# Kernel tuning notes

Measured on AMD Instinct MI355X. Metric: run time of the kernel, lower is better.

The kernel has to match this reference:

```python
import jax, jax.numpy as jnp
import numpy as np

B_SZ, SEQ, D_IN, D_ST, D_OUT = 16, 8192, 128, 128, 128


def setup_inputs() -> dict:
    key = jax.random.key(0)
    ku, ka, kb, kc, kd = jax.random.split(key, 5)
    u = jax.random.normal(ku, (B_SZ, SEQ, D_IN), dtype=jnp.float32)
    # A scaled to spectral radius ~0.9 so the long recurrence stays stable
    A = jax.random.normal(ka, (D_ST, D_ST), dtype=jnp.float32) * (0.9 / np.sqrt(D_ST))
    B = jax.random.normal(kb, (D_ST, D_IN), dtype=jnp.float32) * (1.0 / np.sqrt(D_IN))
    C = jax.random.normal(kc, (D_OUT, D_ST), dtype=jnp.float32) * (1.0 / np.sqrt(D_ST))
    D = jax.random.normal(kd, (D_OUT, D_IN), dtype=jnp.float32) * (1.0 / np.sqrt(D_IN))
    return {"u": u, "A": A, "B": B, "C": C, "D": D}


def reference(u, A, B, C, D):
    # x_t = x_{t-1} A^T + u_t B^T ; y_t = x_t C^T + u_t D^T ; x_0 = 0
    batch = u.shape[0]
    state0 = jnp.zeros((batch, A.shape[0]), dtype=u.dtype)

    def step(state, u_t):  # state: [B, S_dim], u_t: [B, D_in]
        new_state = state @ A.T + u_t @ B.T
        y = new_state @ C.T + u_t @ D.T
        return new_state, y

    u_t_first = jnp.swapaxes(u, 0, 1)  # [SEQ, B, D_in]
    _, ys = jax.lax.scan(step, state0, u_t_first)
    return jnp.swapaxes(ys, 0, 1)  # [B, SEQ, D_out]
```

## Files before the change

### kernel.cpp

```cpp
#include <hip/hip_runtime.h>


#define SEQ 8192
#define BS  16
#define DD  128
#define CL  16
#define NC  512
#define GRP 16
#define NG  32

typedef __bf16 bf16t;
typedef __bf16 bf16x8 __attribute__((ext_vector_type(8)));
typedef __bf16 bf16x4 __attribute__((ext_vector_type(4)));
typedef float  f32x4  __attribute__((ext_vector_type(4)));

#define MFMA(a,b,c) __builtin_amdgcn_mfma_f32_16x16x32_bf16(a,b,c,0,0,0)

__device__ __forceinline__ int swz(int b, int j) { return j ^ ((b & 7) << 3); }

struct Frag  { bf16x8 h[4]; bf16x8 l[4]; };
struct FragH { bf16x8 h[4]; };

__device__ __forceinline__ void load_frag_T(const float* __restrict__ src, int lane, int w, Frag& f) {
    int n  = (w << 4) + (lane & 15);
    int kb = ((lane >> 4) & 3) << 3;
#pragma unroll
    for (int q = 0; q < 4; q++) {
        const float* p = src + n * DD + (q << 5) + kb;
#pragma unroll
        for (int e = 0; e < 8; e++) {
            float v = p[e];
            bf16t hh = (bf16t)v;
            f.h[q][e] = hh;
            f.l[q][e] = (bf16t)(v - (float)hh);
        }
    }
}

__device__ __forceinline__ void load_frag_T_h(const float* __restrict__ src, int lane, int w, FragH& f) {
    int n  = (w << 4) + (lane & 15);
    int kb = ((lane >> 4) & 3) << 3;
#pragma unroll
    for (int q = 0; q < 4; q++) {
        const float* p = src + n * DD + (q << 5) + kb;
#pragma unroll
        for (int e = 0; e < 8; e++) f.h[q][e] = (bf16t)p[e];
    }
}

__device__ __forceinline__ void load_frag_N(const float* __restrict__ src, int lane, int w, Frag& f) {
    int n  = (w << 4) + (lane & 15);
    int kb = ((lane >> 4) & 3) << 3;
#pragma unroll
    for (int q = 0; q < 4; q++) {
#pragma unroll
        for (int e = 0; e < 8; e++) {
            float v = src[((q << 5) + kb + e) * DD + n];
            bf16t hh = (bf16t)v;
            f.h[q][e] = hh;
            f.l[q][e] = (bf16t)(v - (float)hh);
        }
    }
}

__device__ __forceinline__ bf16x8 afrag(const bf16t* __restrict__ X, int lane, int q) {
    int b  = lane & 15;
    int j0 = (q << 5) + (((lane >> 4) & 3) << 3);
    return *(const bf16x8*)(X + b * DD + swz(b, j0));
}

__device__ __forceinline__ void put_state(bf16t* __restrict__ H, bf16t* __restrict__ L,
                                          int lane, int w, f32x4 acc) {
    int n = (w << 4) + (lane & 15);
#pragma unroll
    for (int r = 0; r < 4; r++) {
        int b = (((lane >> 4) & 3) << 2) + r;
        float v = acc[r];
        bf16t hh = (bf16t)v;
        H[b * DD + swz(b, n)] = hh;
        L[b * DD + swz(b, n)] = (bf16t)(v - (float)hh);
    }
}

__device__ __forceinline__ void stage_rows(const float* __restrict__ src, long rs,
                                           bf16t* __restrict__ H, bf16t* __restrict__ L, int tid) {
    int b  = tid >> 5;
    int j0 = (tid & 31) << 2;
    float4 v = *(const float4*)(src + (long)b * rs + j0);
    float vv[4] = { v.x, v.y, v.z, v.w };
    bf16x4 h, l;
#pragma unroll
    for (int e = 0; e < 4; e++) {
        bf16t hh = (bf16t)vv[e];
        h[e] = hh;
        l[e] = (bf16t)(vv[e] - (float)hh);
    }
    *(bf16x4*)(H + b * DD + swz(b, j0)) = h;
    *(bf16x4*)(L + b * DD + swz(b, j0)) = l;
}

__device__ __forceinline__ void write_u_h(bf16t* __restrict__ H, int b_, int j0_, float4 v) {
    float vv[4] = { v.x, v.y, v.z, v.w };
    bf16x4 h;
#pragma unroll
    for (int e = 0; e < 4; e++) h[e] = (bf16t)vv[e];
    *(bf16x4*)(H + b_ * DD + swz(b_, j0_)) = h;
}

__device__ __forceinline__ f32x4 load_accfrag(const float* __restrict__ src, int lane, int w) {
    int n = (w << 4) + (lane & 15);
    f32x4 a;
#pragma unroll
    for (int r = 0; r < 4; r++) {
        int b = (((lane >> 4) & 3) << 2) + r;
        a[r] = src[b * DD + n];
    }
    return a;
}

__device__ __forceinline__ void store_accfrag(float* __restrict__ dst, int lane, int w,
                                              f32x4 a, long rs) {
    int n = (w << 4) + (lane & 15);
#pragma unroll
    for (int r = 0; r < 4; r++) {
        int b = (((lane >> 4) & 3) << 2) + r;
        dst[(long)b * rs + n] = a[r];
    }
}

__global__ __launch_bounds__(128) void k_prepGH(const float* __restrict__ A,
                                                const float* __restrict__ B,
                                                const float* __restrict__ C,
                                                const float* __restrict__ D,
                                                float* __restrict__ Gm, float* __restrict__ Hm) {
    int sel = blockIdx.x >> 7, r = blockIdx.x & 127, j = threadIdx.x;
    const float* R = sel ? B : A;
    float s = 0.f;
#pragma unroll 8
    for (int m = 0; m < 128; m++) s = fmaf(C[r * 128 + m], R[m * 128 + j], s);
    if (sel) Hm[r * 128 + j] = s + D[r * 128 + j];
    else     Gm[r * 128 + j] = s;
}

__global__ __launch_bounds__(512, 4) void k_chunk(const float* __restrict__ u,
                                                  const float* __restrict__ A,
                                                  const float* __restrict__ Bm,
                                                  float* __restrict__ E,
                                                  float* __restrict__ P) {
    __shared__ __align__(16) bf16t Xh[2][BS * DD], Xl[2][BS * DD];
    __shared__ __align__(16) bf16t Uh[2][BS * DD];
    int tid = threadIdx.x, lane = tid & 63, w = tid >> 6;
    bool ident = blockIdx.x < 8;
    int g2 = blockIdx.x, c = blockIdx.x - 8;

    Frag fA; FragH fB;
    load_frag_T(A, lane, w, fA);
    if (!ident) load_frag_T_h(Bm, lane, w, fB);

    for (int i = tid; i < BS * DD; i += 512) {
        int b = i >> 7, j = swz(b, i & 127);
        Xh[0][i] = (bf16t)((ident && j == g2 * 16 + b) ? 1.f : 0.f);
        Xl[0][i] = (bf16t)0.f;
    }
    const float* ubase = u + (long)c * CL * DD;
    int b_ = tid >> 5, j0_ = (tid & 31) << 2;
    if (!ident) {
        float4 v0 = *(const float4*)(ubase + (long)b_ * SEQ * DD + j0_);
        write_u_h(Uh[0], b_, j0_, v0);
    }
    __syncthreads();

    int p = 0;
    f32x4 acc = {0.f, 0.f, 0.f, 0.f};
    for (int i = 0; i < CL; i++) {
        float4 un = {0, 0, 0, 0};
        if (!ident && i + 1 < CL)
            un = *(const float4*)(ubase + (long)b_ * SEQ * DD + (i + 1) * DD + j0_);
        f32x4 ax = {0,0,0,0}, ax2 = {0,0,0,0};
#pragma unroll
        for (int q = 0; q < 4; q++) {
            bf16x8 xh = afrag(Xh[p], lane, q), xl = afrag(Xl[p], lane, q);
            ax  = MFMA(xh, fA.h[q], ax);
            ax2 = MFMA(xl, fA.h[q], ax2);
            ax2 = MFMA(xh, fA.l[q], ax2);
            if (!ident) {
                bf16x8 uh = afrag(Uh[i & 1], lane, q);
                ax = MFMA(uh, fB.h[q], ax);
            }
        }
        acc = ax + ax2;
        if (i + 1 < CL) {
            put_state(Xh[p ^ 1], Xl[p ^ 1], lane, w, acc);
            if (!ident) write_u_h(Uh[(i + 1) & 1], b_, j0_, un);
            __syncthreads();
            p ^= 1;
        }
    }
    if (!ident) store_accfrag(E + (long)c * BS * DD, lane, w, acc, DD);
    else        store_accfrag(P + (long)g2 * 16 * DD, lane, w, acc, DD);
}

__global__ __launch_bounds__(512) void k_group(const float* __restrict__ E,
                                               const float* __restrict__ P,
                                               float* __restrict__ E2,
                                               float* __restrict__ Pg) {
    __shared__ __align__(16) bf16t Xh[2][BS * DD], Xl[2][BS * DD];
    int tid = threadIdx.x, lane = tid & 63, w = tid >> 6;
    bool ident = blockIdx.x >= NG;
    int g2 = blockIdx.x - NG;
    Frag fP;
    load_frag_N(P, lane, w, fP);
    for (int i = tid; i < BS * DD; i += 512) {
        int b = i >> 7, j = swz(b, i & 127);
        Xh[0][i] = (bf16t)((ident && j == g2 * 16 + b) ? 1.f : 0.f);
        Xl[0][i] = (bf16t)0.f;
    }
    __syncthreads();
    int p = 0, g = blockIdx.x;
    f32x4 acc = {0.f, 0.f, 0.f, 0.f};
    for (int r = 0; r < GRP; r++) {
        f32x4 a1 = {0.f,0.f,0.f,0.f}, a2 = {0.f,0.f,0.f,0.f};
        if (!ident) a1 = load_accfrag(E + (long)(g * GRP + r) * BS * DD, lane, w);
#pragma unroll
        for (int q = 0; q < 4; q++) {
            bf16x8 xh = afrag(Xh[p], lane, q), xl = afrag(Xl[p], lane, q);
            a1 = MFMA(xh, fP.h[q], a1);
            a2 = MFMA(xl, fP.h[q], a2);
            a1 = MFMA(xh, fP.l[q], a1);
        }
        acc = a1 + a2;
        if (r + 1 < GRP) {
            put_state(Xh[p ^ 1], Xl[p ^ 1], lane, w, acc);
            __syncthreads();
            p ^= 1;
        }
    }
    if (!ident) store_accfrag(E2 + (long)g * BS * DD, lane, w, acc, DD);
    else        store_accfrag(Pg + (long)g2 * 16 * DD, lane, w, acc, DD);
}

__global__ __launch_bounds__(512) void k_top(const float* __restrict__ E2,
                                             const float* __restrict__ Pg,
                                             float* __restrict__ S2) {
    __shared__ __align__(16) bf16t Xh[2][BS * DD], Xl[2][BS * DD];
    int tid = threadIdx.x, lane = tid & 63, w = tid >> 6;
    Frag fP;
    load_frag_N(Pg, lane, w, fP);
    for (int i = tid; i < BS * DD; i += 512) {
        Xh[0][i] = (bf16t)0.f;
        Xl[0][i] = (bf16t)0.f;
    }
    __syncthreads();
    int p = 0;
    f32x4 T = {0.f, 0.f, 0.f, 0.f};
    f32x4 e2 = load_accfrag(E2, lane, w);
    for (int g = 0; g < NG; g++) {
        store_accfrag(S2 + (long)g * BS * DD, lane, w, T, DD);
        if (g + 1 == NG) break;
        f32x4 e2n = load_accfrag(E2 + (long)(g + 1) * BS * DD, lane, w);
        f32x4 a1 = e2, a2 = {0.f,0.f,0.f,0.f};
#pragma unroll
        for (int q = 0; q < 4; q++) {
            bf16x8 xh = afrag(Xh[p], lane, q), xl = afrag(Xl[p], lane, q);
            a1 = MFMA(xh, fP.h[q], a1);
            a2 = MFMA(xl, fP.h[q], a2);
            a1 = MFMA(xh, fP.l[q], a1);
        }
        T = a1 + a2;
        put_state(Xh[p ^ 1], Xl[p ^ 1], lane, w, T);
        __syncthreads();
        p ^= 1;
        e2 = e2n;
    }
}

__global__ __launch_bounds__(512) void k_fix(float* __restrict__ E,
                                             const float* __restrict__ P,
                                             const float* __restrict__ S2) {
    __shared__ __align__(16) bf16t Xh[2][BS * DD], Xl[2][BS * DD];
    int tid = threadIdx.x, lane = tid & 63, w = tid >> 6;
    int g = blockIdx.x;
    Frag fP;
    load_frag_N(P, lane, w, fP);
    stage_rows(S2 + (long)g * BS * DD, DD, Xh[0], Xl[0], tid);
    f32x4 T = load_accfrag(S2 + (long)g * BS * DD, lane, w);
    __syncthreads();
    int p = 0;
    for (int r = 0; r < GRP; r++) {
        long c = (long)(g * GRP + r) * BS * DD;
        if (r + 1 == GRP) { store_accfrag(E + c, lane, w, T, DD); break; }
        f32x4 a1 = load_accfrag(E + c, lane, w);
        store_accfrag(E + c, lane, w, T, DD);
        f32x4 a2 = {0.f,0.f,0.f,0.f};
#pragma unroll
        for (int q = 0; q < 4; q++) {
            bf16x8 xh = afrag(Xh[p], lane, q), xl = afrag(Xl[p], lane, q);
            a1 = MFMA(xh, fP.h[q], a1);
            a2 = MFMA(xl, fP.h[q], a2);
            a1 = MFMA(xh, fP.l[q], a1);
        }
        T = a1 + a2;
        put_state(Xh[p ^ 1], Xl[p ^ 1], lane, w, T);
        __syncthreads();
        p ^= 1;
    }
}

__global__ __launch_bounds__(512, 4) void k_main(const float* __restrict__ u,
                                                 const float* __restrict__ A,
                                                 const float* __restrict__ Bm,
                                                 const float* __restrict__ Gm,
                                                 const float* __restrict__ Hm,
                                                 const float* __restrict__ S,
                                                 float* __restrict__ out) {
    __shared__ __align__(16) bf16t Xh[2][BS * DD], Xl[2][BS * DD];
    __shared__ __align__(16) bf16t Uh[2][BS * DD];
    int tid = threadIdx.x, lane = tid & 63, w = tid >> 6;
    Frag fA; FragH fB, fG, fH;
    load_frag_T(A, lane, w, fA);
    load_frag_T_h(Bm, lane, w, fB);
    load_frag_T_h(Gm, lane, w, fG);
    load_frag_T_h(Hm, lane, w, fH);
    int c = blockIdx.x;
    const float* ubase = u + (long)c * CL * DD;
    int b_ = tid >> 5, j0_ = (tid & 31) << 2;
    stage_rows(S + (long)c * BS * DD, DD, Xh[0], Xl[0], tid);
    {
        float4 v0 = *(const float4*)(ubase + (long)b_ * SEQ * DD + j0_);
        write_u_h(Uh[0], b_, j0_, v0);
    }
    __syncthreads();
    int p = 0;
    for (int i = 0; i < CL; i++) {
        float4 un = {0, 0, 0, 0};
        if (i + 1 < CL)
            un = *(const float4*)(ubase + (long)b_ * SEQ * DD + (i + 1) * DD + j0_);
        f32x4 ax = {0,0,0,0}, ax2 = {0,0,0,0};
        f32x4 ay = {0,0,0,0}, ay2 = {0,0,0,0};
#pragma unroll
        for (int q = 0; q < 4; q++) {
            bf16x8 xh = afrag(Xh[p], lane, q), xl = afrag(Xl[p], lane, q);
            bf16x8 uh = afrag(Uh[i & 1], lane, q);
            ax  = MFMA(xh, fA.h[q], ax);
            ax  = MFMA(uh, fB.h[q], ax);
            ax2 = MFMA(xl, fA.h[q], ax2);
            ax2 = MFMA(xh, fA.l[q], ax2);
            ay  = MFMA(xh, fG.h[q], ay);
            ay  = MFMA(uh, fH.h[q], ay);
            ay2 = MFMA(xl, fG.h[q], ay2);
        }
        f32x4 xnew = ax + ax2;
        if (i + 1 < CL) {
            put_state(Xh[p ^ 1], Xl[p ^ 1], lane, w, xnew);
            write_u_h(Uh[(i + 1) & 1], b_, j0_, un);
        }
        f32x4 y = ay + ay2;
        store_accfrag(out + ((long)c * CL + i) * DD, lane, w, y, (long)SEQ * DD);
        if (i + 1 < CL) {
            __syncthreads();
            p ^= 1;
        }
    }
}

extern "C" void kernel_launch(void* const* d_in, const int* in_sizes, int n_in,
                              void* d_out, int out_size, void* d_ws, size_t ws_size,
                              hipStream_t stream) {
    (void)in_sizes; (void)n_in; (void)out_size; (void)ws_size;
    const float* u = (const float*)d_in[0];
    const float* A = (const float*)d_in[1];
    const float* B = (const float*)d_in[2];
    const float* C = (const float*)d_in[3];
    const float* D = (const float*)d_in[4];
    float* out = (float*)d_out;
    float* ws  = (float*)d_ws;
    float* Gm = ws;
    float* Hm = Gm + 16384;
    float* P  = Hm + 16384;
    float* Pg = P  + 16384;
    float* E  = Pg + 16384;
    float* E2 = E  + 1048576;
    float* S2 = E2 + 65536;
    dim3 blk(512);
    k_prepGH<<<256, 128, 0, stream>>>(A, B, C, D, Gm, Hm);
    k_chunk<<<NC + 8, blk, 0, stream>>>(u, A, B, E, P);
    k_group<<<NG + 8, blk, 0, stream>>>(E, P, E2, Pg);
    k_top  <<<1,      blk, 0, stream>>>(E2, Pg, S2);
    k_fix  <<<NG,     blk, 0, stream>>>(E, P, S2);
    k_main <<<NC,     blk, 0, stream>>>(u, A, B, Gm, Hm, E, out);
}
```

Measured before the change: 137.1 us.

## Rewrite chunked scan with single-wave MFMA recurrences and producer/consumer warps

Replaces the 512-thread kernels with 64/128-thread kernels in which one wave holds all of A (or P) in registers as transposed fragments. It computes the whole 128x16 state per step with A as the MFMA A-operand. A second wave stages u into LDS and, in pass2, emits outputs from C and D directly instead of the precomputed G=CA and H=CB+D. The prepGH kernel is removed. The aim is to cut the per-step barrier cost across 8 waves and the redundant compensation MFMAs (fewer hi/lo terms). In exchange the per-block work is serialized on a single wave, register use is very high, and occupancy is lower.

```diff
diff --git a/kernel.cpp b/kernel.cpp
--- a/kernel.cpp
+++ b/kernel.cpp
@@ -2,7 +2,6 @@
 
 
 #define SEQ 8192
-#define BS  16
 #define DD  128
 #define CL  16
 #define NC  512
@@ -11,355 +10,406 @@
 
 typedef __bf16 bf16t;
 typedef __bf16 bf16x8 __attribute__((ext_vector_type(8)));
-typedef __bf16 bf16x4 __attribute__((ext_vector_type(4)));
 typedef float  f32x4  __attribute__((ext_vector_type(4)));
+typedef unsigned int u32;
+typedef u32 u32x2 __attribute__((ext_vector_type(2)));
+typedef u32 u32x4 __attribute__((ext_vector_type(4)));
 
 #define MFMA(a,b,c) __builtin_amdgcn_mfma_f32_16x16x32_bf16(a,b,c,0,0,0)
 
-__device__ __forceinline__ int swz(int b, int j) { return j ^ ((b & 7) << 3); }
-
-struct Frag  { bf16x8 h[4]; bf16x8 l[4]; };
-struct FragH { bf16x8 h[4]; };
-
-__device__ __forceinline__ void load_frag_T(const float* __restrict__ src, int lane, int w, Frag& f) {
-    int n  = (w << 4) + (lane & 15);
-    int kb = ((lane >> 4) & 3) << 3;
+__device__ __forceinline__ u32 pkbf(float a, float b) {
+    u32 ha = (u32)__builtin_bit_cast(unsigned short, (bf16t)a);
+    u32 hb = (u32)__builtin_bit_cast(unsigned short, (bf16t)b);
+    return ha | (hb << 16);
+}
+__device__ __forceinline__ float lo_f(u32 p) { return __uint_as_float(p << 16); }
+__device__ __forceinline__ float hi_f(u32 p) { return __uint_as_float(p & 0xffff0000u); }
+
+__device__ __forceinline__ bf16x8 ld8(const float* __restrict__ p) {
+    float4 a = *(const float4*)p;
+    float4 b = *(const float4*)(p + 4);
+    bf16x8 r;
+    r[0]=(bf16t)a.x; r[1]=(bf16t)a.y; r[2]=(bf16t)a.z; r[3]=(bf16t)a.w;
+    r[4]=(bf16t)b.x; r[5]=(bf16t)b.y; r[6]=(bf16t)b.z; r[7]=(bf16t)b.w;
+    return r;
+}
+__device__ __forceinline__ void ld8hl(const float* __restrict__ p, bf16x8& h, bf16x8& l) {
+    float4 a = *(const float4*)p;
+    float4 b = *(const float4*)(p + 4);
+    float v[8] = {a.x,a.y,a.z,a.w,b.x,b.y,b.z,b.w};
+#pragma unroll
+    for (int e = 0; e < 8; e++) { bf16t hh = (bf16t)v[e]; h[e] = hh; l[e] = (bf16t)(v[e] - (float)hh); }
+}
+
+__device__ __forceinline__ void load_fragsH(const float* __restrict__ M, int g, int c, bf16x8 f[8][4]) {
+#pragma unroll
+    for (int mt = 0; mt < 8; mt++)
+#pragma unroll
+        for (int q = 0; q < 4; q++)
+            f[mt][q] = ld8(M + (mt*16 + c)*DD + q*32 + g*8);
+}
+__device__ __forceinline__ void load_fragsHL(const float* __restrict__ M, int g, int c,
+                                             bf16x8 fh[8][4], bf16x8 fl[8][4]) {
+#pragma unroll
+    for (int mt = 0; mt < 8; mt++)
+#pragma unroll
+        for (int q = 0; q < 4; q++)
+            ld8hl(M + (mt*16 + c)*DD + q*32 + g*8, fh[mt][q], fl[mt][q]);
+}
+
+__device__ __forceinline__ void x_write(u32* __restrict__ XHp, u32* __restrict__ XLp,
+                                        const f32x4* acc, int g, int c) {
+#pragma unroll
+    for (int mt = 0; mt < 8; mt++) {
+        f32x4 a = acc[mt];
+        u32 h0 = pkbf(a[0], a[1]), h1 = pkbf(a[2], a[3]);
+        float l0 = a[0] - lo_f(h0), l1 = a[1] - hi_f(h0);
+        float l2 = a[2] - lo_f(h1), l3 = a[3] - hi_f(h1);
+        u32 q0 = pkbf(l0, l1), q1 = pkbf(l2, l3);
+        int base = ((2*mt + (g >> 1))*16 + c)*4 + 2*(g & 1);
+        *(u32x2*)(XHp + base) = u32x2{h0, h1};
+        *(u32x2*)(XLp + base) = u32x2{q0, q1};
+    }
+}
+__device__ __forceinline__ void x_read(const u32* __restrict__ Xp, int g, int c, bf16x8* f) {
 #pragma unroll
     for (int q = 0; q < 4; q++) {
-        const float* p = src + n * DD + (q << 5) + kb;
-#pragma unroll
-        for (int e = 0; e < 8; e++) {
-            float v = p[e];
-            bf16t hh = (bf16t)v;
-            f.h[q][e] = hh;
-            f.l[q][e] = (bf16t)(v - (float)hh);
-        }
-    }
-}
-
-__device__ __forceinline__ void load_frag_T_h(const float* __restrict__ src, int lane, int w, FragH& f) {
-    int n  = (w << 4) + (lane & 15);
-    int kb = ((lane >> 4) & 3) << 3;
-#pragma unroll
-    for (int q = 0; q < 4; q++) {
-        const float* p = src + n * DD + (q << 5) + kb;
-#pragma unroll
-        for (int e = 0; e < 8; e++) f.h[q][e] = (bf16t)p[e];
-    }
-}
-
-__device__ __forceinline__ void load_frag_N(const float* __restrict__ src, int lane, int w, Frag& f) {
-    int n  = (w << 4) + (lane & 15);
-    int kb = ((lane >> 4) & 3) << 3;
-#pragma unroll
-    for (int q = 0; q < 4; q++) {
-#pragma unroll
-        for (int e = 0; e < 8; e++) {
-            float v = src[((q << 5) + kb + e) * DD + n];
-            bf16t hh = (bf16t)v;
-            f.h[q][e] = hh;
-            f.l[q][e] = (bf16t)(v - (float)hh);
-        }
-    }
-}
-
-__device__ __forceinline__ bf16x8 afrag(const bf16t* __restrict__ X, int lane, int q) {
-    int b  = lane & 15;
-    int j0 = (q << 5) + (((lane >> 4) & 3) << 3);
-    return *(const bf16x8*)(X + b * DD + swz(b, j0));
-}
-
-__device__ __forceinline__ void put_state(bf16t* __restrict__ H, bf16t* __restrict__ L,
-                                          int lane, int w, f32x4 acc) {
-    int n = (w << 4) + (lane & 15);
-#pragma unroll
-    for (int r = 0; r < 4; r++) {
-        int b = (((lane >> 4) & 3) << 2) + r;
-        float v = acc[r];
-        bf16t hh = (bf16t)v;
-        H[b * DD + swz(b, n)] = hh;
-        L[b * DD + swz(b, n)] = (bf16t)(v - (float)hh);
-    }
-}
-
-__device__ __forceinline__ void stage_rows(const float* __restrict__ src, long rs,
-                                           bf16t* __restrict__ H, bf16t* __restrict__ L, int tid) {
-    int b  = tid >> 5;
-    int j0 = (tid & 31) << 2;
-    float4 v = *(const float4*)(src + (long)b * rs + j0);
-    float vv[4] = { v.x, v.y, v.z, v.w };
-    bf16x4 h, l;
-#pragma unroll
-    for (int e = 0; e < 4; e++) {
-        bf16t hh = (bf16t)vv[e];
-        h[e] = hh;
-        l[e] = (bf16t)(vv[e] - (float)hh);
-    }
-    *(bf16x4*)(H + b * DD + swz(b, j0)) = h;
-    *(bf16x4*)(L + b * DD + swz(b, j0)) = l;
-}
-
-__device__ __forceinline__ void write_u_h(bf16t* __restrict__ H, int b_, int j0_, float4 v) {
-    float vv[4] = { v.x, v.y, v.z, v.w };
-    bf16x4 h;
-#pragma unroll
-    for (int e = 0; e < 4; e++) h[e] = (bf16t)vv[e];
-    *(bf16x4*)(H + b_ * DD + swz(b_, j0_)) = h;
-}
-
-__device__ __forceinline__ f32x4 load_accfrag(const float* __restrict__ src, int lane, int w) {
-    int n = (w << 4) + (lane & 15);
-    f32x4 a;
-#pragma unroll
-    for (int r = 0; r < 4; r++) {
-        int b = (((lane >> 4) & 3) << 2) + r;
-        a[r] = src[b * DD + n];
-    }
-    return a;
-}
-
-__device__ __forceinline__ void store_accfrag(float* __restrict__ dst, int lane, int w,
-                                              f32x4 a, long rs) {
-    int n = (w << 4) + (lane & 15);
-#pragma unroll
-    for (int r = 0; r < 4; r++) {
-        int b = (((lane >> 4) & 3) << 2) + r;
-        dst[(long)b * rs + n] = a[r];
-    }
-}
-
-__global__ __launch_bounds__(128) void k_prepGH(const float* __restrict__ A,
-                                                const float* __restrict__ B,
-                                                const float* __restrict__ C,
-                                                const float* __restrict__ D,
-                                                float* __restrict__ Gm, float* __restrict__ Hm) {
-    int sel = blockIdx.x >> 7, r = blockIdx.x & 127, j = threadIdx.x;
-    const float* R = sel ? B : A;
-    float s = 0.f;
-#pragma unroll 8
-    for (int m = 0; m < 128; m++) s = fmaf(C[r * 128 + m], R[m * 128 + j], s);
-    if (sel) Hm[r * 128 + j] = s + D[r * 128 + j];
-    else     Gm[r * 128 + j] = s;
-}
-
-__global__ __launch_bounds__(512, 4) void k_chunk(const float* __restrict__ u,
-                                                  const float* __restrict__ A,
+        u32x4 v = *(const u32x4*)(Xp + ((4*q + g)*16 + c)*4);
+        f[q] = __builtin_bit_cast(bf16x8, v);
+    }
+}
+
+__device__ __forceinline__ void stage_u(const float* __restrict__ u, long c, int t,
+                                        int lane, u32* __restrict__ U) {
+    int cb = lane >> 2, dq = lane & 3;
+    const float* p = u + (long)cb*SEQ*DD + ((long)c*CL + t)*DD + dq*32;
+    float v[32];
+#pragma unroll
+    for (int i = 0; i < 8; i++) *(float4*)(v + 4*i) = *(const float4*)(p + 4*i);
+    u32 pk[16];
+#pragma unroll
+    for (int k = 0; k < 16; k++) pk[k] = pkbf(v[2*k], v[2*k+1]);
+#pragma unroll
+    for (int g = 0; g < 4; g++)
+        *(u32x4*)(U + (dq*256 + g*64 + cb*4)) = u32x4{pk[4*g], pk[4*g+1], pk[4*g+2], pk[4*g+3]};
+}
+__device__ __forceinline__ void u_read(const u32* __restrict__ U, int lane, bf16x8* f) {
+#pragma unroll
+    for (int q = 0; q < 4; q++)
+        f[q] = __builtin_bit_cast(bf16x8, *(const u32x4*)(U + q*256 + lane*4));
+}
+
+__device__ __forceinline__ void seed_ident(u32* __restrict__ XHp, u32* __restrict__ XLp,
+                                           int w, int lane) {
+    for (int i = lane; i < 1024; i += 64) { XHp[i] = 0u; XLp[i] = 0u; }
+    int g = (lane >> 4) & 3, c = lane & 15;
+    if (g == 0) {
+        int row = 16*w + c;
+        int rp = row >> 1;
+        XHp[((rp >> 2)*16 + c)*4 + (rp & 3)] = (row & 1) ? 0x3f800000u : 0x00003f80u;
+    }
+}
+
+__global__ __launch_bounds__(128, 1) void k_pass1(const float* __restrict__ u,
+                                                  const float* __restrict__ Am,
                                                   const float* __restrict__ Bm,
                                                   float* __restrict__ E,
-                                                  float* __restrict__ P) {
-    __shared__ __align__(16) bf16t Xh[2][BS * DD], Xl[2][BS * DD];
-    __shared__ __align__(16) bf16t Uh[2][BS * DD];
-    int tid = threadIdx.x, lane = tid & 63, w = tid >> 6;
-    bool ident = blockIdx.x < 8;
-    int g2 = blockIdx.x, c = blockIdx.x - 8;
-
-    Frag fA; FragH fB;
-    load_frag_T(A, lane, w, fA);
-    if (!ident) load_frag_T_h(Bm, lane, w, fB);
-
-    for (int i = tid; i < BS * DD; i += 512) {
-        int b = i >> 7, j = swz(b, i & 127);
-        Xh[0][i] = (bf16t)((ident && j == g2 * 16 + b) ? 1.f : 0.f);
-        Xl[0][i] = (bf16t)0.f;
-    }
-    const float* ubase = u + (long)c * CL * DD;
-    int b_ = tid >> 5, j0_ = (tid & 31) << 2;
-    if (!ident) {
-        float4 v0 = *(const float4*)(ubase + (long)b_ * SEQ * DD + j0_);
-        write_u_h(Uh[0], b_, j0_, v0);
-    }
-    __syncthreads();
-
-    int p = 0;
-    f32x4 acc = {0.f, 0.f, 0.f, 0.f};
-    for (int i = 0; i < CL; i++) {
-        float4 un = {0, 0, 0, 0};
-        if (!ident && i + 1 < CL)
-            un = *(const float4*)(ubase + (long)b_ * SEQ * DD + (i + 1) * DD + j0_);
-        f32x4 ax = {0,0,0,0}, ax2 = {0,0,0,0};
+                                                  float* __restrict__ Pm) {
+    __shared__ u32 XH[2][1024], XL[2][1024], UB[3][1024];
+    int tid = threadIdx.x, lane = tid & 63, wid = tid >> 6;
+    int g = (lane >> 4) & 3, c = lane & 15;
+    int bid = blockIdx.x;
+    if (bid < NC) {
+        long ch = bid;
+        if (wid == 0) {
+            bf16x8 fA[8][4], fB[8][4];
+            load_fragsH(Am, g, c, fA);
+            load_fragsH(Bm, g, c, fB);
+            f32x4 acc[8];
+            __syncthreads();
+            for (int t = 0; t < CL; t++) {
+                bf16x8 uf[4];
+                u_read(UB[t % 3], lane, uf);
+                bf16x8 xh[4], xl[4];
+                if (t > 0) { x_read(XH[t & 1], g, c, xh); x_read(XL[t & 1], g, c, xl); }
+#pragma unroll
+                for (int mt = 0; mt < 8; mt++) {
+                    f32x4 a = {0.f, 0.f, 0.f, 0.f};
+#pragma unroll
+                    for (int q = 0; q < 4; q++) a = MFMA(fB[mt][q], uf[q], a);
+                    if (t > 0) {
+#pragma unroll
+                        for (int q = 0; q < 4; q++) {
+                            a = MFMA(fA[mt][q], xh[q], a);
+                            a = MFMA(fA[mt][q], xl[q], a);
+                        }
+                    }
+                    acc[mt] = a;
+                }
+                if (t < CL - 1) x_write(XH[(t+1) & 1], XL[(t+1) & 1], acc, g, c);
+                __syncthreads();
+            }
+#pragma unroll
+            for (int mt = 0; mt < 8; mt++)
+                *(f32x4*)(E + (ch*8 + mt)*256 + lane*4) = acc[mt];
+        } else {
+            stage_u(u, ch, 0, lane, UB[0]);
+            __syncthreads();
+            for (int t = 0; t < CL; t++) {
+                if (t + 1 < CL) stage_u(u, ch, t + 1, lane, UB[(t+1) % 3]);
+                __syncthreads();
+            }
+        }
+    } else {
+        int w = (bid - NC)*2 + wid;
+        bf16x8 fA[8][4];
+        load_fragsH(Am, g, c, fA);
+        u32* xhp = XH[wid]; u32* xlp = XL[wid];
+        seed_ident(xhp, xlp, w, lane);
+        f32x4 acc[8];
+        for (int t = 0; t < CL; t++) {
+            bf16x8 xh[4], xl[4];
+            x_read(xhp, g, c, xh); x_read(xlp, g, c, xl);
+#pragma unroll
+            for (int mt = 0; mt < 8; mt++) {
+                f32x4 a = {0.f, 0.f, 0.f, 0.f};
+#pragma unroll
+                for (int q = 0; q < 4; q++) {
+                    a = MFMA(fA[mt][q], xh[q], a);
+                    a = MFMA(fA[mt][q], xl[q], a);
+                }
+                acc[mt] = a;
+            }
+            x_write(xhp, xlp, acc, g, c);
+        }
+#pragma unroll
+        for (int mt = 0; mt < 8; mt++)
+#pragma unroll
+            for (int r = 0; r < 4; r++)
+                Pm[(mt*16 + 4*g + r)*DD + 16*w + c] = acc[mt][r];
+    }
+}
+
+__global__ __launch_bounds__(64, 1) void k_group(const float* __restrict__ E,
+                                                 const float* __restrict__ Pm,
+                                                 float* __restrict__ E2,
+                                                 float* __restrict__ Pg) {
+    __shared__ u32 XH[2][1024], XL[2][1024];
+    int lane = threadIdx.x & 63;
+    int g = (lane >> 4) & 3, c = lane & 15;
+    int bid = blockIdx.x;
+    bf16x8 fPh[8][4], fPl[8][4];
+    load_fragsHL(Pm, g, c, fPh, fPl);
+    if (bid < NG) {
+        f32x4 T[8];
+        for (int r = 0; r < GRP; r++) {
+            long cc = (long)bid*GRP + r;
+            f32x4 e[8];
+#pragma unroll
+            for (int mt = 0; mt < 8; mt++) e[mt] = *(const f32x4*)(E + (cc*8 + mt)*256 + lane*4);
+            if (r > 0) {
+                bf16x8 xh[4], xl[4];
+                x_read(XH[r & 1], g, c, xh); x_read(XL[r & 1], g, c, xl);
+#pragma unroll
+                for (int mt = 0; mt < 8; mt++) {
+                    f32x4 a = e[mt];
+#pragma unroll
+                    for (int q = 0; q < 4; q++) {
+                        a = MFMA(fPh[mt][q], xh[q], a);
+                        a = MFMA(fPh[mt][q], xl[q], a);
+                        a = MFMA(fPl[mt][q], xh[q], a);
+                    }
+                    T[mt] = a;
+                }
+            } else {
+#pragma unroll
+                for (int mt = 0; mt < 8; mt++) T[mt] = e[mt];
+            }
+            if (r < GRP - 1) x_write(XH[(r+1) & 1], XL[(r+1) & 1], T, g, c);
+        }
+#pragma unroll
+        for (int mt = 0; mt < 8; mt++)
+            *(f32x4*)(E2 + ((long)bid*8 + mt)*256 + lane*4) = T[mt];
+    } else {
+        int w = bid - NG;
+        seed_ident(XH[0], XL[0], w, lane);
+        f32x4 T[8];
+        for (int r = 0; r < GRP; r++) {
+            bf16x8 xh[4], xl[4];
+            x_read(XH[r & 1], g, c, xh); x_read(XL[r & 1], g, c, xl);
+#pragma unroll
+            for (int mt = 0; mt < 8; mt++) {
+                f32x4 a = {0.f, 0.f, 0.f, 0.f};
+#pragma unroll
+                for (int q = 0; q < 4; q++) {
+                    a = MFMA(fPh[mt][q], xh[q], a);
+                    a = MFMA(fPh[mt][q], xl[q], a);
+                    a = MFMA(fPl[mt][q], xh[q], a);
+                }
+                T[mt] = a;
+            }
+            x_write(XH[(r+1) & 1], XL[(r+1) & 1], T, g, c);
+        }
+#pragma unroll
+        for (int mt = 0; mt < 8; mt++)
+#pragma unroll
+            for (int r = 0; r < 4; r++)
+                Pg[(mt*16 + 4*g + r)*DD + 16*w + c] = T[mt][r];
+    }
+}
+
+__global__ __launch_bounds__(64, 1) void k_top(const float* __restrict__ E2,
+                                               const float* __restrict__ Pgm,
+                                               float* __restrict__ S2) {
+    __shared__ u32 XH[2][1024], XL[2][1024];
+    int lane = threadIdx.x & 63;
+    int g = (lane >> 4) & 3, c = lane & 15;
+    bf16x8 fPh[8][4], fPl[8][4];
+    load_fragsHL(Pgm, g, c, fPh, fPl);
+    f32x4 T[8];
+#pragma unroll
+    for (int mt = 0; mt < 8; mt++) T[mt] = f32x4{0.f, 0.f, 0.f, 0.f};
+    for (int gg = 0; gg < NG; gg++) {
+#pragma unroll
+        for (int mt = 0; mt < 8; mt++)
+            *(f32x4*)(S2 + ((long)gg*8 + mt)*256 + lane*4) = T[mt];
+        if (gg == NG - 1) break;
+        f32x4 e[8];
+#pragma unroll
+        for (int mt = 0; mt < 8; mt++) e[mt] = *(const f32x4*)(E2 + ((long)gg*8 + mt)*256 + lane*4);
+        if (gg > 0) {
+            bf16x8 xh[4], xl[4];
+            x_read(XH[gg & 1], g, c, xh); x_read(XL[gg & 1], g, c, xl);
+#pragma unroll
+            for (int mt = 0; mt < 8; mt++) {
+                f32x4 a = e[mt];
+#pragma unroll
+                for (int q = 0; q < 4; q++) {
+                    a = MFMA(fPh[mt][q], xh[q], a);
+                    a = MFMA(fPh[mt][q], xl[q], a);
+                    a = MFMA(fPl[mt][q], xh[q], a);
+                }
+                T[mt] = a;
+            }
+        } else {
+#pragma unroll
+            for (int mt = 0; mt < 8; mt++) T[mt] = e[mt];
+        }
+        x_write(XH[(gg+1) & 1], XL[(gg+1) & 1], T, g, c);
+    }
+}
+
+__global__ __launch_bounds__(64, 1) void k_fix(float* __restrict__ E,
+                                               const float* __restrict__ Pm,
+                                               const float* __restrict__ S2) {
+    __shared__ u32 XH[2][1024], XL[2][1024];
+    int lane = threadIdx.x & 63;
+    int g = (lane >> 4) & 3, c = lane & 15;
+    int gr = blockIdx.x;
+    bf16x8 fPh[8][4], fPl[8][4];
+    load_fragsHL(Pm, g, c, fPh, fPl);
+    f32x4 T[8];
+#pragma unroll
+    for (int mt = 0; mt < 8; mt++) T[mt] = *(const f32x4*)(S2 + ((long)gr*8 + mt)*256 + lane*4);
+    x_write(XH[0], XL[0], T, g, c);
+    for (int r = 0; r < GRP; r++) {
+        long cc = (long)gr*GRP + r;
+        f32x4 e[8];
+#pragma unroll
+        for (int mt = 0; mt < 8; mt++) e[mt] = *(const f32x4*)(E + (cc*8 + mt)*256 + lane*4);
+#pragma unroll
+        for (int mt = 0; mt < 8; mt++)
+            *(f32x4*)(E + (cc*8 + mt)*256 + lane*4) = T[mt];
+        if (r == GRP - 1) break;
+        bf16x8 xh[4], xl[4];
+        x_read(XH[r & 1], g, c, xh); x_read(XL[r & 1], g, c, xl);
+#pragma unroll
+        for (int mt = 0; mt < 8; mt++) {
+            f32x4 a = e[mt];
+#pragma unroll
+            for (int q = 0; q < 4; q++) {
+                a = MFMA(fPh[mt][q], xh[q], a);
+                a = MFMA(fPh[mt][q], xl[q], a);
+                a = MFMA(fPl[mt][q], xh[q], a);
+            }
+            T[mt] = a;
+        }
+        x_write(XH[(r+1) & 1], XL[(r+1) & 1], T, g, c);
+    }
+}
+
+__device__ __forceinline__ void y_emit(const bf16x8 (&fC)[8][4], const bf16x8 (&fD)[8][4],
+                                       const u32* __restrict__ XHp, const u32* __restrict__ UBp,
+                                       int g, int c, int lane, long tg, float* __restrict__ out) {
+    bf16x8 xh[4]; x_read(XHp, g, c, xh);
+    bf16x8 uf[4]; u_read(UBp, lane, uf);
+#pragma unroll
+    for (int mt = 0; mt < 8; mt++) {
+        f32x4 a = {0.f, 0.f, 0.f, 0.f};
 #pragma unroll
         for (int q = 0; q < 4; q++) {
-            bf16x8 xh = afrag(Xh[p], lane, q), xl = afrag(Xl[p], lane, q);
-            ax  = MFMA(xh, fA.h[q], ax);
-            ax2 = MFMA(xl, fA.h[q], ax2);
-            ax2 = MFMA(xh, fA.l[q], ax2);
-            if (!ident) {
-                bf16x8 uh = afrag(Uh[i & 1], lane, q);
-                ax = MFMA(uh, fB.h[q], ax);
-            }
-        }
-        acc = ax + ax2;
-        if (i + 1 < CL) {
-            put_state(Xh[p ^ 1], Xl[p ^ 1], lane, w, acc);
-            if (!ident) write_u_h(Uh[(i + 1) & 1], b_, j0_, un);
+            a = MFMA(fC[mt][q], xh[q], a);
+            a = MFMA(fD[mt][q], uf[q], a);
+        }
+        *(f32x4*)(out + (long)c*SEQ*DD + tg*DD + mt*16 + 4*g) = a;
+    }
+}
+
+__global__ __launch_bounds__(128, 1) void k_pass2(const float* __restrict__ u,
+                                                  const float* __restrict__ Am,
+                                                  const float* __restrict__ Bm,
+                                                  const float* __restrict__ Cm,
+                                                  const float* __restrict__ Dm,
+                                                  const float* __restrict__ S,
+                                                  float* __restrict__ out) {
+    __shared__ u32 XH[2][1024], XL[2][1024], UB[3][1024];
+    int tid = threadIdx.x, lane = tid & 63, wid = tid >> 6;
+    int g = (lane >> 4) & 3, c = lane & 15;
+    long ch = blockIdx.x;
+    if (wid == 0) {
+        bf16x8 fA[8][4], fB[8][4];
+        load_fragsH(Am, g, c, fA);
+        load_fragsH(Bm, g, c, fB);
+        {
+            f32x4 s0[8];
+#pragma unroll
+            for (int mt = 0; mt < 8; mt++) s0[mt] = *(const f32x4*)(S + (ch*8 + mt)*256 + lane*4);
+            x_write(XH[0], XL[0], s0, g, c);
+        }
+        __syncthreads();
+        for (int t = 0; t < CL; t++) {
+            bf16x8 uf[4]; u_read(UB[t % 3], lane, uf);
+            bf16x8 xh[4], xl[4];
+            x_read(XH[t & 1], g, c, xh); x_read(XL[t & 1], g, c, xl);
+            f32x4 acc[8];
+#pragma unroll
+            for (int mt = 0; mt < 8; mt++) {
+                f32x4 a = {0.f, 0.f, 0.f, 0.f};
+#pragma unroll
+                for (int q = 0; q < 4; q++) a = MFMA(fB[mt][q], uf[q], a);
+#pragma unroll
+                for (int q = 0; q < 4; q++) {
+                    a = MFMA(fA[mt][q], xh[q], a);
+                    a = MFMA(fA[mt][q], xl[q], a);
+                }
+                acc[mt] = a;
+            }
+            x_write(XH[(t+1) & 1], XL[(t+1) & 1], acc, g, c);
             __syncthreads();
-            p ^= 1;
-        }
-    }
-    if (!ident) store_accfrag(E + (long)c * BS * DD, lane, w, acc, DD);
-    else        store_accfrag(P + (long)g2 * 16 * DD, lane, w, acc, DD);
-}
-
-__global__ __launch_bounds__(512) void k_group(const float* __restrict__ E,
-                                               const float* __restrict__ P,
-                                               float* __restrict__ E2,
-                                               float* __restrict__ Pg) {
-    __shared__ __align__(16) bf16t Xh[2][BS * DD], Xl[2][BS * DD];
-    int tid = threadIdx.x, lane = tid & 63, w = tid >> 6;
-    bool ident = blockIdx.x >= NG;
-    int g2 = blockIdx.x - NG;
-    Frag fP;
-    load_frag_N(P, lane, w, fP);
-    for (int i = tid; i < BS * DD; i += 512) {
-        int b = i >> 7, j = swz(b, i & 127);
-        Xh[0][i] = (bf16t)((ident && j == g2 * 16 + b) ? 1.f : 0.f);
-        Xl[0][i] = (bf16t)0.f;
-    }
-    __syncthreads();
-    int p = 0, g = blockIdx.x;
-    f32x4 acc = {0.f, 0.f, 0.f, 0.f};
-    for (int r = 0; r < GRP; r++) {
-        f32x4 a1 = {0.f,0.f,0.f,0.f}, a2 = {0.f,0.f,0.f,0.f};
-        if (!ident) a1 = load_accfrag(E + (long)(g * GRP + r) * BS * DD, lane, w);
-#pragma unroll
-        for (int q = 0; q < 4; q++) {
-            bf16x8 xh = afrag(Xh[p], lane, q), xl = afrag(Xl[p], lane, q);
-            a1 = MFMA(xh, fP.h[q], a1);
-            a2 = MFMA(xl, fP.h[q], a2);
-            a1 = MFMA(xh, fP.l[q], a1);
-        }
-        acc = a1 + a2;
-        if (r + 1 < GRP) {
-            put_state(Xh[p ^ 1], Xl[p ^ 1], lane, w, acc);
+        }
+    } else {
+        bf16x8 fC[8][4], fD[8][4];
+        load_fragsH(Cm, g, c, fC);
+        load_fragsH(Dm, g, c, fD);
+        stage_u(u, ch, 0, lane, UB[0]);
+        __syncthreads();
+        for (int t = 0; t < CL; t++) {
+            if (t + 1 < CL) stage_u(u, ch, t + 1, lane, UB[(t+1) % 3]);
+            if (t > 0)
+                y_emit(fC, fD, XH[t & 1], UB[(t-1) % 3], g, c, lane, ch*CL + (t-1), out);
             __syncthreads();
-            p ^= 1;
-        }
-    }
-    if (!ident) store_accfrag(E2 + (long)g * BS * DD, lane, w, acc, DD);
-    else        store_accfrag(Pg + (long)g2 * 16 * DD, lane, w, acc, DD);
-}
-
-__global__ __launch_bounds__(512) void k_top(const float* __restrict__ E2,
-                                             const float* __restrict__ Pg,
-                                             float* __restrict__ S2) {
-    __shared__ __align__(16) bf16t Xh[2][BS * DD], Xl[2][BS * DD];
-    int tid = threadIdx.x, lane = tid & 63, w = tid >> 6;
-    Frag fP;
-    load_frag_N(Pg, lane, w, fP);
-    for (int i = tid; i < BS * DD; i += 512) {
-        Xh[0][i] = (bf16t)0.f;
-        Xl[0][i] = (bf16t)0.f;
-    }
-    __syncthreads();
-    int p = 0;
-    f32x4 T = {0.f, 0.f, 0.f, 0.f};
-    f32x4 e2 = load_accfrag(E2, lane, w);
-    for (int g = 0; g < NG; g++) {
-        store_accfrag(S2 + (long)g * BS * DD, lane, w, T, DD);
-        if (g + 1 == NG) break;
-        f32x4 e2n = load_accfrag(E2 + (long)(g + 1) * BS * DD, lane, w);
-        f32x4 a1 = e2, a2 = {0.f,0.f,0.f,0.f};
-#pragma unroll
-        for (int q = 0; q < 4; q++) {
-            bf16x8 xh = afrag(Xh[p], lane, q), xl = afrag(Xl[p], lane, q);
-            a1 = MFMA(xh, fP.h[q], a1);
-            a2 = MFMA(xl, fP.h[q], a2);
-            a1 = MFMA(xh, fP.l[q], a1);
-        }
-        T = a1 + a2;
-        put_state(Xh[p ^ 1], Xl[p ^ 1], lane, w, T);
-        __syncthreads();
-        p ^= 1;
-        e2 = e2n;
-    }
-}
-
-__global__ __launch_bounds__(512) void k_fix(float* __restrict__ E,
-                                             const float* __restrict__ P,
-                                             const float* __restrict__ S2) {
-    __shared__ __align__(16) bf16t Xh[2][BS * DD], Xl[2][BS * DD];
-    int tid = threadIdx.x, lane = tid & 63, w = tid >> 6;
-    int g = blockIdx.x;
-    Frag fP;
-    load_frag_N(P, lane, w, fP);
-    stage_rows(S2 + (long)g * BS * DD, DD, Xh[0], Xl[0], tid);
-    f32x4 T = load_accfrag(S2 + (long)g * BS * DD, lane, w);
-    __syncthreads();
-    int p = 0;
-    for (int r = 0; r < GRP; r++) {
-        long c = (long)(g * GRP + r) * BS * DD;
-        if (r + 1 == GRP) { store_accfrag(E + c, lane, w, T, DD); break; }
-        f32x4 a1 = load_accfrag(E + c, lane, w);
-        store_accfrag(E + c, lane, w, T, DD);
-        f32x4 a2 = {0.f,0.f,0.f,0.f};
-#pragma unroll
-        for (int q = 0; q < 4; q++) {
-            bf16x8 xh = afrag(Xh[p], lane, q), xl = afrag(Xl[p], lane, q);
-            a1 = MFMA(xh, fP.h[q], a1);
-            a2 = MFMA(xl, fP.h[q], a2);
-            a1 = MFMA(xh, fP.l[q], a1);
-        }
-        T = a1 + a2;
-        put_state(Xh[p ^ 1], Xl[p ^ 1], lane, w, T);
-        __syncthreads();
-        p ^= 1;
-    }
-}
-
-__global__ __launch_bounds__(512, 4) void k_main(const float* __restrict__ u,
-                                                 const float* __restrict__ A,
-                                                 const float* __restrict__ Bm,
-                                                 const float* __restrict__ Gm,
-                                                 const float* __restrict__ Hm,
-                                                 const float* __restrict__ S,
-                                                 float* __restrict__ out) {
-    __shared__ __align__(16) bf16t Xh[2][BS * DD], Xl[2][BS * DD];
-    __shared__ __align__(16) bf16t Uh[2][BS * DD];
-    int tid = threadIdx.x, lane = tid & 63, w = tid >> 6;
-    Frag fA; FragH fB, fG, fH;
-    load_frag_T(A, lane, w, fA);
-    load_frag_T_h(Bm, lane, w, fB);
-    load_frag_T_h(Gm, lane, w, fG);
-    load_frag_T_h(Hm, lane, w, fH);
-    int c = blockIdx.x;
-    const float* ubase = u + (long)c * CL * DD;
-    int b_ = tid >> 5, j0_ = (tid & 31) << 2;
-    stage_rows(S + (long)c * BS * DD, DD, Xh[0], Xl[0], tid);
-    {
-        float4 v0 = *(const float4*)(ubase + (long)b_ * SEQ * DD + j0_);
-        write_u_h(Uh[0], b_, j0_, v0);
-    }
-    __syncthreads();
-    int p = 0;
-    for (int i = 0; i < CL; i++) {
-        float4 un = {0, 0, 0, 0};
-        if (i + 1 < CL)
-            un = *(const float4*)(ubase + (long)b_ * SEQ * DD + (i + 1) * DD + j0_);
-        f32x4 ax = {0,0,0,0}, ax2 = {0,0,0,0};
-        f32x4 ay = {0,0,0,0}, ay2 = {0,0,0,0};
-#pragma unroll
-        for (int q = 0; q < 4; q++) {
-            bf16x8 xh = afrag(Xh[p], lane, q), xl = afrag(Xl[p], lane, q);
-            bf16x8 uh = afrag(Uh[i & 1], lane, q);
-            ax  = MFMA(xh, fA.h[q], ax);
-            ax  = MFMA(uh, fB.h[q], ax);
-            ax2 = MFMA(xl, fA.h[q], ax2);
-            ax2 = MFMA(xh, fA.l[q], ax2);
-            ay  = MFMA(xh, fG.h[q], ay);
-            ay  = MFMA(uh, fH.h[q], ay);
-            ay2 = MFMA(xl, fG.h[q], ay2);
-        }
-        f32x4 xnew = ax + ax2;
-        if (i + 1 < CL) {
-            put_state(Xh[p ^ 1], Xl[p ^ 1], lane, w, xnew);
-            write_u_h(Uh[(i + 1) & 1], b_, j0_, un);
-        }
-        f32x4 y = ay + ay2;
-        store_accfrag(out + ((long)c * CL + i) * DD, lane, w, y, (long)SEQ * DD);
-        if (i + 1 < CL) {
-            __syncthreads();
-            p ^= 1;
-        }
+        }
+        y_emit(fC, fD, XH[CL & 1], UB[(CL-1) % 3], g, c, lane, ch*CL + (CL-1), out);
     }
 }
 
@@ -374,18 +424,14 @@
     const float* D = (const float*)d_in[4];
     float* out = (float*)d_out;
     float* ws  = (float*)d_ws;
-    float* Gm = ws;
-    float* Hm = Gm + 16384;
-    float* P  = Hm + 16384;
-    float* Pg = P  + 16384;
-    float* E  = Pg + 16384;
-    float* E2 = E  + 1048576;
-    float* S2 = E2 + 65536;
-    dim3 blk(512);
-    k_prepGH<<<256, 128, 0, stream>>>(A, B, C, D, Gm, Hm);
-    k_chunk<<<NC + 8, blk, 0, stream>>>(u, A, B, E, P);
-    k_group<<<NG + 8, blk, 0, stream>>>(E, P, E2, Pg);
-    k_top  <<<1,      blk, 0, stream>>>(E2, Pg, S2);
-    k_fix  <<<NG,     blk, 0, stream>>>(E, P, S2);
-    k_main <<<NC,     blk, 0, stream>>>(u, A, B, Gm, Hm, E, out);
-}
+    float* E  = ws;
+    float* E2 = E  + (long)NC*2048;
+    float* S2 = E2 + (long)NG*2048;
+    float* Pm = S2 + (long)NG*2048;
+    float* Pg = Pm + 16384;
+    k_pass1<<<NC + 4, 128, 0, stream>>>(u, A, B, E, Pm);
+    k_group<<<NG + 8, 64, 0, stream>>>(E, Pm, E2, Pg);
+    k_top  <<<1,      64, 0, stream>>>(E2, Pg, S2);
+    k_fix  <<<NG,     64, 0, stream>>>(E, Pm, S2);
+    k_pass2<<<NC,     128, 0, stream>>>(u, A, B, C, D, E, out);
+}
```

Result: slower. 254.2 us (+85.4%).
